# Performance work log

Measured on AMD Instinct MI355X. Metric: run time of the kernel, lower is better.

Reference implementation:

```python
import jax, jax.numpy as jnp
import numpy as np

B, C, HID, H, W = 4, 64, 64, 64, 64


def setup_inputs() -> dict:
    key = jax.random.key(0)
    ks = jax.random.split(key, 9)
    s_in = 1.0 / np.sqrt(C)
    return {
        "x": jax.random.normal(ks[0], (B, C, H, W), dtype=jnp.float32),
        "Wq": jax.random.normal(ks[1], (HID, C), dtype=jnp.float32) * s_in,
        "bq": jnp.zeros((HID,), dtype=jnp.float32),
        "Wk": jax.random.normal(ks[2], (HID, C), dtype=jnp.float32) * s_in,
        "bk": jnp.zeros((HID,), dtype=jnp.float32),
        "Wv": jax.random.normal(ks[3], (C, C), dtype=jnp.float32) * s_in,
        "bv": jnp.zeros((C,), dtype=jnp.float32),
        "Wo": jax.random.normal(ks[4], (1, C), dtype=jnp.float32) * s_in,
        "bo": jnp.zeros((1,), dtype=jnp.float32),
    }


def reference(x, Wq, bq, Wk, bk, Wv, bv, Wo, bo):
    b, c, h, w = x.shape
    n = h * w
    xf = x.reshape(b, c, n)                                   # [B,C,N]
    q = jnp.einsum('dc,bcn->bnd', Wq, xf) + bq                # [B,N,HID]
    k = jnp.einsum('dc,bcn->bdn', Wk, xf) + bk[None, :, None]  # [B,HID,N]
    v = jnp.einsum('ec,bcn->bne', Wv, xf) + bv                # [B,N,C]
    scale = 1.0 / jnp.sqrt(jnp.asarray(k.shape[1], x.dtype))
    attn = jax.nn.softmax(jnp.einsum('bnd,bdm->bnm', q, k) * scale, axis=-1)
    out = jnp.einsum('bnm,bme->bne', attn, v)                 # [B,N,C]
    out = out.transpose(0, 2, 1).reshape(b, c, h, w)
    y = jnp.einsum('oc,bchw->bohw', Wo, out) + bo[None, :, None, None]
    return jax.nn.sigmoid(y)
```

## Files before the change

kernel.cpp:

```cpp
#include <hip/hip_runtime.h>
#include <math.h>

#define NB 4
#define NN 4096
#define QSCALE 0.1803368801f

#define KS 8
#define KPB 512
#define KPW 128
#define NTILES 8
#define NG 8

typedef __bf16 bf16x8 __attribute__((ext_vector_type(8)));
typedef float f32x4 __attribute__((ext_vector_type(4)));

union BF8 { unsigned short u[8]; bf16x8 v; uint4 q; };

static __device__ inline unsigned short f2bf(float f) {
    union { float f; unsigned u; } v; v.f = f;
    unsigned r = v.u + 0x7fffu + ((v.u >> 16) & 1u);
    return (unsigned short)(r >> 16);
}

__global__ __launch_bounds__(256) void prep_mfma(
    const float* __restrict__ x,
    const float* __restrict__ Wq, const float* __restrict__ bq,
    const float* __restrict__ Wk, const float* __restrict__ bk,
    const float* __restrict__ Wv, const float* __restrict__ bv,
    const float* __restrict__ Wo,
    unsigned short* __restrict__ Qb, unsigned short* __restrict__ Kb,
    float* __restrict__ VW)
{
    __shared__ float xt[64 * 65];
    __shared__ float wve_s[64];
    unsigned short* rows = (unsigned short*)xt;

    const int blk = blockIdx.x;
    const int b = blk >> 6;
    const int n0 = (blk & 63) << 6;
    const int tid = threadIdx.x;
    const int wid = tid >> 6, lane = tid & 63;
    const int lg = lane >> 4, ll = lane & 15;

    const float* xb = x + (size_t)b * 64 * NN;
    #pragma unroll
    for (int it = 0; it < 16; ++it) {
        int idx = it * 256 + tid;
        int c = idx >> 6, n = idx & 63;
        xt[c * 65 + n] = xb[(size_t)c * NN + n0 + n];
    }
    if (tid < 64) {
        float a = 0.f;
        for (int e = 0; e < 64; ++e) a = fmaf(Wo[e], Wv[e * 64 + tid], a);
        wve_s[tid] = a;
    }
    float cv = 0.f;
    for (int e = 0; e < 64; ++e) cv = fmaf(Wo[e], bv[e], cv);
    __syncthreads();

    BF8 a0, a1;
    #pragma unroll
    for (int j = 0; j < 8; ++j) {
        a0.v[j] = (__bf16)xt[(lg * 8 + j) * 65 + wid * 16 + ll];
        a1.v[j] = (__bf16)xt[(32 + lg * 8 + j) * 65 + wid * 16 + ll];
    }

    {
        int nrel = wid * 16 + (lane >> 2);
        int part = lane & 3;
        float a = 0.f;
        #pragma unroll
        for (int j = 0; j < 16; ++j)
            a = fmaf(wve_s[part * 16 + j], xt[(part * 16 + j) * 65 + nrel], a);
        a += __shfl_xor(a, 1);
        a += __shfl_xor(a, 2);
        if (part == 0) VW[(size_t)b * NN + n0 + nrel] = a + cv;
    }

    f32x4 qacc[4];
    #pragma unroll
    for (int ct = 0; ct < 4; ++ct) {
        const float* wr = Wq + (ct * 16 + ll) * 64;
        float4 f0 = *(const float4*)(wr + lg * 8);
        float4 f1 = *(const float4*)(wr + lg * 8 + 4);
        float4 f2 = *(const float4*)(wr + 32 + lg * 8);
        float4 f3 = *(const float4*)(wr + 32 + lg * 8 + 4);
        BF8 w0, w1;
        w0.v[0] = (__bf16)f0.x; w0.v[1] = (__bf16)f0.y; w0.v[2] = (__bf16)f0.z; w0.v[3] = (__bf16)f0.w;
        w0.v[4] = (__bf16)f1.x; w0.v[5] = (__bf16)f1.y; w0.v[6] = (__bf16)f1.z; w0.v[7] = (__bf16)f1.w;
        w1.v[0] = (__bf16)f2.x; w1.v[1] = (__bf16)f2.y; w1.v[2] = (__bf16)f2.z; w1.v[3] = (__bf16)f2.w;
        w1.v[4] = (__bf16)f3.x; w1.v[5] = (__bf16)f3.y; w1.v[6] = (__bf16)f3.z; w1.v[7] = (__bf16)f3.w;
        f32x4 acc = {0.f, 0.f, 0.f, 0.f};
        acc = __builtin_amdgcn_mfma_f32_16x16x32_bf16(a0.v, w0.v, acc, 0, 0, 0);
        acc = __builtin_amdgcn_mfma_f32_16x16x32_bf16(a1.v, w1.v, acc, 0, 0, 0);
        qacc[ct] = acc;
    }
    __syncthreads();

    #pragma unroll
    for (int ct = 0; ct < 4; ++ct) {
        float bias = bq[ct * 16 + ll];
        #pragma unroll
        for (int r = 0; r < 4; ++r) {
            int n = wid * 16 + lg * 4 + r;
            rows[n * 72 + ct * 16 + ll] = f2bf((qacc[ct][r] + bias) * QSCALE);
        }
    }
    __syncthreads();
    {
        int n = tid >> 2, qq = tid & 3;
        const uint4* src = (const uint4*)&rows[n * 72 + qq * 16];
        uint4 v0 = src[0], v1 = src[1];
        uint4* dst = (uint4*)(Qb + ((size_t)b * NN + n0 + n) * 64 + qq * 16);
        dst[0] = v0; dst[1] = v1;
    }

    f32x4 kacc[4];
    #pragma unroll
    for (int ct = 0; ct < 4; ++ct) {
        const float* wr = Wk + (ct * 16 + ll) * 64;
        float4 f0 = *(const float4*)(wr + lg * 8);
        float4 f1 = *(const float4*)(wr + lg * 8 + 4);
        float4 f2 = *(const float4*)(wr + 32 + lg * 8);
        float4 f3 = *(const float4*)(wr + 32 + lg * 8 + 4);
        BF8 w0, w1;
        w0.v[0] = (__bf16)f0.x; w0.v[1] = (__bf16)f0.y; w0.v[2] = (__bf16)f0.z; w0.v[3] = (__bf16)f0.w;
        w0.v[4] = (__bf16)f1.x; w0.v[5] = (__bf16)f1.y; w0.v[6] = (__bf16)f1.z; w0.v[7] = (__bf16)f1.w;
        w1.v[0] = (__bf16)f2.x; w1.v[1] = (__bf16)f2.y; w1.v[2] = (__bf16)f2.z; w1.v[3] = (__bf16)f2.w;
        w1.v[4] = (__bf16)f3.x; w1.v[5] = (__bf16)f3.y; w1.v[6] = (__bf16)f3.z; w1.v[7] = (__bf16)f3.w;
        f32x4 acc = {0.f, 0.f, 0.f, 0.f};
        acc = __builtin_amdgcn_mfma_f32_16x16x32_bf16(a0.v, w0.v, acc, 0, 0, 0);
        acc = __builtin_amdgcn_mfma_f32_16x16x32_bf16(a1.v, w1.v, acc, 0, 0, 0);
        kacc[ct] = acc;
    }
    __syncthreads();
    #pragma unroll
    for (int ct = 0; ct < 4; ++ct) {
        float bias = bk[ct * 16 + ll];
        #pragma unroll
        for (int r = 0; r < 4; ++r) {
            int n = wid * 16 + lg * 4 + r;
            rows[n * 72 + ct * 16 + ll] = f2bf(kacc[ct][r] + bias);
        }
    }
    __syncthreads();
    {
        int n = tid >> 2, qq = tid & 3;
        const uint4* src = (const uint4*)&rows[n * 72 + qq * 16];
        uint4 v0 = src[0], v1 = src[1];
        uint4* dst = (uint4*)(Kb + ((size_t)b * NN + n0 + n) * 64 + qq * 16);
        dst[0] = v0; dst[1] = v1;
    }
}

__global__ __launch_bounds__(256) void attn_mfma(
    const unsigned short* __restrict__ Qb, const unsigned short* __restrict__ Kb,
    const float* __restrict__ VW, float2* __restrict__ P2)
{
    __shared__ float vws[KPB];
    const int blk = blockIdx.x;
    const int ks = blk & (KS - 1);
    const int t = blk >> 3;
    const int b = t >> 5;
    const int q0 = (t & 31) << 7;
    const int tid = threadIdx.x;
    const int wid = tid >> 6, lane = tid & 63;
    const int lg = lane >> 4, ll = lane & 15;

    for (int i = tid; i < KPB; i += 256)
        vws[i] = VW[(size_t)b * NN + ks * KPB + i];
    __syncthreads();

    bf16x8 qfa[NG], qfb[NG];
    #pragma unroll
    for (int g = 0; g < NG; ++g) {
        const unsigned short* qp = Qb + ((size_t)b * NN + q0 + g * 16 + ll) * 64 + lg * 8;
        qfa[g] = *(const bf16x8*)qp;
        qfb[g] = *(const bf16x8*)(qp + 32);
    }
    const unsigned short* kp =
        Kb + ((size_t)b * NN + ks * KPB + wid * KPW + ll) * 64 + lg * 8;

    float Zg[NG], Ag[NG];
    #pragma unroll
    for (int g = 0; g < NG; ++g) { Zg[g] = 0.f; Ag[g] = 0.f; }

    bf16x8 ka0 = *(const bf16x8*)kp;
    bf16x8 ka1 = *(const bf16x8*)(kp + 32);

    #pragma unroll
    for (int kt = 0; kt < NTILES; ++kt) {
        const bf16x8 c0 = ka0, c1 = ka1;
        const int nx = (kt + 1 < NTILES) ? kt + 1 : kt;
        const unsigned short* np = kp + (size_t)nx * (16 * 64);
        ka0 = *(const bf16x8*)np;
        ka1 = *(const bf16x8*)(np + 32);

        const float4 vv = *(const float4*)&vws[wid * KPW + kt * 16 + lg * 4];
        #pragma unroll
        for (int g = 0; g < NG; ++g) {
            f32x4 acc = {0.f, 0.f, 0.f, 0.f};
            acc = __builtin_amdgcn_mfma_f32_16x16x32_bf16(c0, qfa[g], acc, 0, 0, 0);
            acc = __builtin_amdgcn_mfma_f32_16x16x32_bf16(c1, qfb[g], acc, 0, 0, 0);
            float e0 = __builtin_amdgcn_exp2f(acc[0]);
            float e1 = __builtin_amdgcn_exp2f(acc[1]);
            float e2 = __builtin_amdgcn_exp2f(acc[2]);
            float e3 = __builtin_amdgcn_exp2f(acc[3]);
            Zg[g] += (e0 + e1) + (e2 + e3);
            Ag[g] += fmaf(e0, vv.x, fmaf(e1, vv.y, fmaf(e2, vv.z, e3 * vv.w)));
        }
    }

    #pragma unroll
    for (int g = 0; g < NG; ++g) {
        Zg[g] += __shfl_xor(Zg[g], 16);
        Zg[g] += __shfl_xor(Zg[g], 32);
        Ag[g] += __shfl_xor(Ag[g], 16);
        Ag[g] += __shfl_xor(Ag[g], 32);
    }
    const int r = ks * 4 + wid;
    float Z1 = (lg == 0) ? Zg[0] : (lg == 1) ? Zg[1] : (lg == 2) ? Zg[2] : Zg[3];
    float A1 = (lg == 0) ? Ag[0] : (lg == 1) ? Ag[1] : (lg == 2) ? Ag[2] : Ag[3];
    float Z2 = (lg == 0) ? Zg[4] : (lg == 1) ? Zg[5] : (lg == 2) ? Zg[6] : Zg[7];
    float A2 = (lg == 0) ? Ag[4] : (lg == 1) ? Ag[5] : (lg == 2) ? Ag[6] : Ag[7];
    size_t base = ((size_t)r << 14) + ((size_t)b << 12) + q0;
    P2[base + lg * 16 + ll]       = make_float2(Z1, A1);
    P2[base + (lg + 4) * 16 + ll] = make_float2(Z2, A2);
}

__global__ __launch_bounds__(256) void combine_kernel(
    const float2* __restrict__ P2, const float* __restrict__ bo,
    float* __restrict__ out)
{
    int i = blockIdx.x * 256 + threadIdx.x;
    float Z = 0.f, A = 0.f;
    #pragma unroll
    for (int r = 0; r < 32; ++r) {
        float2 p = P2[((size_t)r << 14) + i];
        Z += p.x; A += p.y;
    }
    float y = A / Z + bo[0];
    out[i] = 1.f / (1.f + __expf(-y));
}

extern "C" void kernel_launch(void* const* d_in, const int* in_sizes, int n_in,
                              void* d_out, int out_size, void* d_ws, size_t ws_size,
                              hipStream_t stream)
{
    const float* x  = (const float*)d_in[0];
    const float* Wq = (const float*)d_in[1];
    const float* bq = (const float*)d_in[2];
    const float* Wk = (const float*)d_in[3];
    const float* bk = (const float*)d_in[4];
    const float* Wv = (const float*)d_in[5];
    const float* bv = (const float*)d_in[6];
    const float* Wo = (const float*)d_in[7];
    const float* bo = (const float*)d_in[8];
    float* out = (float*)d_out;

    unsigned short* Qb = (unsigned short*)d_ws;
    unsigned short* Kb = Qb + (size_t)NB * NN * 64;
    float* VW = (float*)(Kb + (size_t)NB * NN * 64);
    float2* P2 = (float2*)(VW + (size_t)NB * NN);

    prep_mfma<<<NB * 64, 256, 0, stream>>>(x, Wq, bq, Wk, bk, Wv, bv, Wo, Qb, Kb, VW);
    attn_mfma<<<NB * 32 * KS, 256, 0, stream>>>(Qb, Kb, VW, P2);
    combine_kernel<<<(NB * NN) / 256, 256, 0, stream>>>(P2, bo, out);
}
```

Baseline: 39.97 us.

## Halve per-block work in all kernels, stage Q in LDS, split Q/K across waves

The prep kernel now handles 32 positions per block, and waves 0-1 compute Q while waves 2-3 compute K in parallel instead of sequentially with extra barriers. The Wo·Wv and Wo·bv reductions are parallelized across threads with shuffles. The attention kernel now takes 64 queries per block instead of 128, so it launches twice as many blocks, and reads Q fragments from LDS instead of holding them in registers. The K-tile software prefetch is dropped and combine uses 64-thread blocks. The aim is more blocks for better CU occupancy and fewer registers, at the cost of reading K from global twice as often and adding LDS reads of Q inside the inner loop.

```diff
diff --git a/kernel.cpp b/kernel.cpp
--- a/kernel.cpp
+++ b/kernel.cpp
@@ -9,7 +9,7 @@
 #define KPB 512
 #define KPW 128
 #define NTILES 8
-#define NG 8
+#define NG 4
 
 typedef __bf16 bf16x8 __attribute__((ext_vector_type(8)));
 typedef float f32x4 __attribute__((ext_vector_type(4)));
@@ -31,56 +31,76 @@
     unsigned short* __restrict__ Qb, unsigned short* __restrict__ Kb,
     float* __restrict__ VW)
 {
-    __shared__ float xt[64 * 65];
+    __shared__ float xt[64 * 33];
     __shared__ float wve_s[64];
-    unsigned short* rows = (unsigned short*)xt;
+    __shared__ unsigned short rows[4 * 16 * 72];
 
     const int blk = blockIdx.x;
-    const int b = blk >> 6;
-    const int n0 = (blk & 63) << 6;
+    const int b = blk >> 7;
+    const int n0 = (blk & 127) << 5;
     const int tid = threadIdx.x;
     const int wid = tid >> 6, lane = tid & 63;
     const int lg = lane >> 4, ll = lane & 15;
 
     const float* xb = x + (size_t)b * 64 * NN;
     #pragma unroll
-    for (int it = 0; it < 16; ++it) {
+    for (int it = 0; it < 8; ++it) {
         int idx = it * 256 + tid;
-        int c = idx >> 6, n = idx & 63;
-        xt[c * 65 + n] = xb[(size_t)c * NN + n0 + n];
-    }
-    if (tid < 64) {
+        int c = idx >> 5, n = idx & 31;
+        xt[c * 33 + n] = xb[(size_t)c * NN + n0 + n];
+    }
+    {
+        int c = tid >> 2, part = tid & 3;
         float a = 0.f;
-        for (int e = 0; e < 64; ++e) a = fmaf(Wo[e], Wv[e * 64 + tid], a);
-        wve_s[tid] = a;
-    }
-    float cv = 0.f;
-    for (int e = 0; e < 64; ++e) cv = fmaf(Wo[e], bv[e], cv);
-    __syncthreads();
-
-    BF8 a0, a1;
-    #pragma unroll
-    for (int j = 0; j < 8; ++j) {
-        a0.v[j] = (__bf16)xt[(lg * 8 + j) * 65 + wid * 16 + ll];
-        a1.v[j] = (__bf16)xt[(32 + lg * 8 + j) * 65 + wid * 16 + ll];
-    }
-
-    {
-        int nrel = wid * 16 + (lane >> 2);
-        int part = lane & 3;
-        float a = 0.f;
-        #pragma unroll
-        for (int j = 0; j < 16; ++j)
-            a = fmaf(wve_s[part * 16 + j], xt[(part * 16 + j) * 65 + nrel], a);
+        #pragma unroll
+        for (int j = 0; j < 16; ++j) {
+            int e = part * 16 + j;
+            a = fmaf(Wo[e], Wv[e * 64 + c], a);
+        }
         a += __shfl_xor(a, 1);
         a += __shfl_xor(a, 2);
+        if (part == 0) wve_s[c] = a;
+    }
+    float cv;
+    {
+        float p = Wo[lane] * bv[lane];
+        #pragma unroll
+        for (int off = 1; off < 64; off <<= 1) p += __shfl_xor(p, off);
+        cv = p;
+    }
+    __syncthreads();
+
+    {
+        int nrel = tid >> 3, part = tid & 7;
+        float a = 0.f;
+        #pragma unroll
+        for (int j = 0; j < 8; ++j) {
+            int c = part * 8 + j;
+            a = fmaf(wve_s[c], xt[c * 33 + nrel], a);
+        }
+        a += __shfl_xor(a, 1);
+        a += __shfl_xor(a, 2);
+        a += __shfl_xor(a, 4);
         if (part == 0) VW[(size_t)b * NN + n0 + nrel] = a + cv;
     }
 
-    f32x4 qacc[4];
+    const int nr = (wid & 1) * 16 + ll;
+    BF8 a0, a1;
+    #pragma unroll
+    for (int j = 0; j < 8; ++j) {
+        a0.v[j] = (__bf16)xt[(lg * 8 + j) * 33 + nr];
+        a1.v[j] = (__bf16)xt[(32 + lg * 8 + j) * 33 + nr];
+    }
+
+    const float* W  = (wid < 2) ? Wq : Wk;
+    const float* bs = (wid < 2) ? bq : bk;
+    unsigned short* Out = (wid < 2) ? Qb : Kb;
+    const float scale = (wid < 2) ? QSCALE : 1.f;
+    unsigned short* myrows = rows + wid * (16 * 72);
+
     #pragma unroll
     for (int ct = 0; ct < 4; ++ct) {
-        const float* wr = Wq + (ct * 16 + ll) * 64;
+        const float* wr = W + (ct * 16 + ll) * 64;
         float4 f0 = *(const float4*)(wr + lg * 8);
         float4 f1 = *(const float4*)(wr + lg * 8 + 4);
         float4 f2 = *(const float4*)(wr + 32 + lg * 8);
@@ -93,62 +113,16 @@
         f32x4 acc = {0.f, 0.f, 0.f, 0.f};
         acc = __builtin_amdgcn_mfma_f32_16x16x32_bf16(a0.v, w0.v, acc, 0, 0, 0);
         acc = __builtin_amdgcn_mfma_f32_16x16x32_bf16(a1.v, w1.v, acc, 0, 0, 0);
-        qacc[ct] = acc;
-    }
-    __syncthreads();
-
-    #pragma unroll
-    for (int ct = 0; ct < 4; ++ct) {
-        float bias = bq[ct * 16 + ll];
-        #pragma unroll
-        for (int r = 0; r < 4; ++r) {
-            int n = wid * 16 + lg * 4 + r;
-            rows[n * 72 + ct * 16 + ll] = f2bf((qacc[ct][r] + bias) * QSCALE);
-        }
-    }
-    __syncthreads();
-    {
-        int n = tid >> 2, qq = tid & 3;
-        const uint4* src = (const uint4*)&rows[n * 72 + qq * 16];
-        uint4 v0 = src[0], v1 = src[1];
-        uint4* dst = (uint4*)(Qb + ((size_t)b * NN + n0 + n) * 64 + qq * 16);
-        dst[0] = v0; dst[1] = v1;
-    }
-
-    f32x4 kacc[4];
-    #pragma unroll
-    for (int ct = 0; ct < 4; ++ct) {
-        const float* wr = Wk + (ct * 16 + ll) * 64;
-        float4 f0 = *(const float4*)(wr + lg * 8);
-        float4 f1 = *(const float4*)(wr + lg * 8 + 4);
-        float4 f2 = *(const float4*)(wr + 32 + lg * 8);
-        float4 f3 = *(const float4*)(wr + 32 + lg * 8 + 4);
-        BF8 w0, w1;
-        w0.v[0] = (__bf16)f0.x; w0.v[1] = (__bf16)f0.y; w0.v[2] = (__bf16)f0.z; w0.v[3] = (__bf16)f0.w;
-        w0.v[4] = (__bf16)f1.x; w0.v[5] = (__bf16)f1.y; w0.v[6] = (__bf16)f1.z; w0.v[7] = (__bf16)f1.w;
-        w1.v[0] = (__bf16)f2.x; w1.v[1] = (__bf16)f2.y; w1.v[2] = (__bf16)f2.z; w1.v[3] = (__bf16)f2.w;
-        w1.v[4] = (__bf16)f3.x; w1.v[5] = (__bf16)f3.y; w1.v[6] = (__bf16)f3.z; w1.v[7] = (__bf16)f3.w;
-        f32x4 acc = {0.f, 0.f, 0.f, 0.f};
-        acc = __builtin_amdgcn_mfma_f32_16x16x32_bf16(a0.v, w0.v, acc, 0, 0, 0);
-        acc = __builtin_amdgcn_mfma_f32_16x16x32_bf16(a1.v, w1.v, acc, 0, 0, 0);
-        kacc[ct] = acc;
-    }
-    __syncthreads();
-    #pragma unroll
-    for (int ct = 0; ct < 4; ++ct) {
-        float bias = bk[ct * 16 + ll];
-        #pragma unroll
-        for (int r = 0; r < 4; ++r) {
-            int n = wid * 16 + lg * 4 + r;
-            rows[n * 72 + ct * 16 + ll] = f2bf(kacc[ct][r] + bias);
-        }
-    }
-    __syncthreads();
-    {
-        int n = tid >> 2, qq = tid & 3;
-        const uint4* src = (const uint4*)&rows[n * 72 + qq * 16];
-        uint4 v0 = src[0], v1 = src[1];
-        uint4* dst = (uint4*)(Kb + ((size_t)b * NN + n0 + n) * 64 + qq * 16);
+        float bias = bs[ct * 16 + ll];
+        #pragma unroll
+        for (int r = 0; r < 4; ++r)
+            myrows[(lg * 4 + r) * 72 + ct * 16 + ll] = f2bf((acc[r] + bias) * scale);
+    }
+    {
+        int n = lane >> 2, c16 = lane & 3;
+        const uint4* sp = (const uint4*)&myrows[n * 72 + c16 * 16];
+        uint4 v0 = sp[0], v1 = sp[1];
+        uint4* dst = (uint4*)(Out + ((size_t)b * NN + n0 + (wid & 1) * 16 + n) * 64 + c16 * 16);
         dst[0] = v0; dst[1] = v1;
     }
 }
@@ -157,27 +131,31 @@
     const unsigned short* __restrict__ Qb, const unsigned short* __restrict__ Kb,
     const float* __restrict__ VW, float2* __restrict__ P2)
 {
+    __shared__ unsigned short qlds[64 * 72];
     __shared__ float vws[KPB];
     const int blk = blockIdx.x;
     const int ks = blk & (KS - 1);
     const int t = blk >> 3;
-    const int b = t >> 5;
-    const int q0 = (t & 31) << 7;
+    const int b = t >> 6;
+    const int q0 = (t & 63) << 6;
     const int tid = threadIdx.x;
     const int wid = tid >> 6, lane = tid & 63;
     const int lg = lane >> 4, ll = lane & 15;
 
+    {
+        const uint4* src = (const uint4*)(Qb + ((size_t)b * NN + q0) * 64);
+        #pragma unroll
+        for (int k = 0; k < 2; ++k) {
+            int idx = tid + k * 256;
+            int row = idx >> 3, c8 = idx & 7;
+            uint4 v = src[idx];
+            *(uint4*)&qlds[row * 72 + c8 * 8] = v;
+        }
+    }
     for (int i = tid; i < KPB; i += 256)
         vws[i] = VW[(size_t)b * NN + ks * KPB + i];
     __syncthreads();
 
-    bf16x8 qfa[NG], qfb[NG];
-    #pragma unroll
-    for (int g = 0; g < NG; ++g) {
-        const unsigned short* qp = Qb + ((size_t)b * NN + q0 + g * 16 + ll) * 64 + lg * 8;
-        qfa[g] = *(const bf16x8*)qp;
-        qfb[g] = *(const bf16x8*)(qp + 32);
-    }
     const unsigned short* kp =
         Kb + ((size_t)b * NN + ks * KPB + wid * KPW + ll) * 64 + lg * 8;
 
@@ -185,23 +163,18 @@
     #pragma unroll
     for (int g = 0; g < NG; ++g) { Zg[g] = 0.f; Ag[g] = 0.f; }
 
-    bf16x8 ka0 = *(const bf16x8*)kp;
-    bf16x8 ka1 = *(const bf16x8*)(kp + 32);
-
     #pragma unroll
     for (int kt = 0; kt < NTILES; ++kt) {
-        const bf16x8 c0 = ka0, c1 = ka1;
-        const int nx = (kt + 1 < NTILES) ? kt + 1 : kt;
-        const unsigned short* np = kp + (size_t)nx * (16 * 64);
-        ka0 = *(const bf16x8*)np;
-        ka1 = *(const bf16x8*)(np + 32);
-
+        const bf16x8 ka0 = *(const bf16x8*)(kp + kt * (16 * 64));
+        const bf16x8 ka1 = *(const bf16x8*)(kp + kt * (16 * 64) + 32);
         const float4 vv = *(const float4*)&vws[wid * KPW + kt * 16 + lg * 4];
         #pragma unroll
         for (int g = 0; g < NG; ++g) {
+            const bf16x8 qa = *(const bf16x8*)&qlds[(g * 16 + ll) * 72 + lg * 8];
+            const bf16x8 qc = *(const bf16x8*)&qlds[(g * 16 + ll) * 72 + 32 + lg * 8];
             f32x4 acc = {0.f, 0.f, 0.f, 0.f};
-            acc = __builtin_amdgcn_mfma_f32_16x16x32_bf16(c0, qfa[g], acc, 0, 0, 0);
-            acc = __builtin_amdgcn_mfma_f32_16x16x32_bf16(c1, qfb[g], acc, 0, 0, 0);
+            acc = __builtin_amdgcn_mfma_f32_16x16x32_bf16(ka0, qa, acc, 0, 0, 0);
+            acc = __builtin_amdgcn_mfma_f32_16x16x32_bf16(ka1, qc, acc, 0, 0, 0);
             float e0 = __builtin_amdgcn_exp2f(acc[0]);
             float e1 = __builtin_amdgcn_exp2f(acc[1]);
             float e2 = __builtin_amdgcn_exp2f(acc[2]);
@@ -219,20 +192,16 @@
         Ag[g] += __shfl_xor(Ag[g], 32);
     }
     const int r = ks * 4 + wid;
-    float Z1 = (lg == 0) ? Zg[0] : (lg == 1) ? Zg[1] : (lg == 2) ? Zg[2] : Zg[3];
-    float A1 = (lg == 0) ? Ag[0] : (lg == 1) ? Ag[1] : (lg == 2) ? Ag[2] : Ag[3];
-    float Z2 = (lg == 0) ? Zg[4] : (lg == 1) ? Zg[5] : (lg == 2) ? Zg[6] : Zg[7];
-    float A2 = (lg == 0) ? Ag[4] : (lg == 1) ? Ag[5] : (lg == 2) ? Ag[6] : Ag[7];
-    size_t base = ((size_t)r << 14) + ((size_t)b << 12) + q0;
-    P2[base + lg * 16 + ll]       = make_float2(Z1, A1);
-    P2[base + (lg + 4) * 16 + ll] = make_float2(Z2, A2);
-}
-
-__global__ __launch_bounds__(256) void combine_kernel(
+    float Zo = (lg == 0) ? Zg[0] : (lg == 1) ? Zg[1] : (lg == 2) ? Zg[2] : Zg[3];
+    float Ao = (lg == 0) ? Ag[0] : (lg == 1) ? Ag[1] : (lg == 2) ? Ag[2] : Ag[3];
+    P2[((size_t)r << 14) + ((size_t)b << 12) + q0 + lane] = make_float2(Zo, Ao);
+}
+
+__global__ __launch_bounds__(64) void combine_kernel(
     const float2* __restrict__ P2, const float* __restrict__ bo,
     float* __restrict__ out)
 {
-    int i = blockIdx.x * 256 + threadIdx.x;
+    int i = blockIdx.x * 64 + threadIdx.x;
     float Z = 0.f, A = 0.f;
     #pragma unroll
     for (int r = 0; r < 32; ++r) {
@@ -263,7 +232,7 @@
     float* VW = (float*)(Kb + (size_t)NB * NN * 64);
     float2* P2 = (float2*)(VW + (size_t)NB * NN);
 
-    prep_mfma<<<NB * 64, 256, 0, stream>>>(x, Wq, bq, Wk, bk, Wv, bv, Wo, Qb, Kb, VW);
-    attn_mfma<<<NB * 32 * KS, 256, 0, stream>>>(Qb, Kb, VW, P2);
-    combine_kernel<<<(NB * NN) / 256, 256, 0, stream>>>(P2, bo, out);
-}
+    prep_mfma<<<NB * 128, 256, 0, stream>>>(x, Wq, bq, Wk, bk, Wv, bv, Wo, Qb, Kb, VW);
+    attn_mfma<<<NB * 64 * KS, 256, 0, stream>>>(Qb, Kb, VW, P2);
+    combine_kernel<<<(NB * NN) / 64, 64, 0, stream>>>(P2, bo, out);
+}
```

Measured after the change: 37.89 us. 5.2% less time.
